# Optimization experiments

Measured on AMD Instinct MI355X. Metric: run time of the kernel, lower is better.

## Reference

```python
import jax, jax.numpy as jnp
import numpy as np

N, E, F_IN, H, T, OUT, ATTR = 20000, 640000, 128, 128, 12, 64, 4


def _glorot(key, shape):
    lim = 1.0 / np.sqrt(shape[0])
    return jax.random.uniform(key, shape, jnp.float32, -lim, lim)


def setup_inputs() -> dict:
    key = jax.random.key(0)
    ks = jax.random.split(key, 48)
    inp = {
        "x": jax.random.normal(ks[0], (N, F_IN, T), jnp.float32),
        "edge_attr": jax.random.uniform(ks[1], (E, ATTR), jnp.float32),
        "edge_index": jax.random.randint(ks[2], (2, E), 0, N, jnp.int32),
    }
    k = 3
    for i, cin in enumerate([F_IN, H]):
        gi = cin + 2 * H
        inp[f"gw{i}"] = _glorot(ks[k], (cin, H)); k += 1
        inp[f"gb{i}"] = jnp.zeros((H,), jnp.float32)
        for g in ["f", "i", "o", "c"]:
            inp[f"w{g}{i}"] = _glorot(ks[k], (gi, H)); k += 1
            inp[f"b{g}{i}"] = jnp.zeros((H,), jnp.float32)
    inp["ow"] = _glorot(ks[k], (H, OUT)); k += 1
    inp["ob"] = jnp.zeros((OUT,), jnp.float32)
    return inp


def _forward(edge_index, x, edge_attr, gw0, gb0, wf0, bf0, wi0, bi0, wo0, bo0, wc0, bc0,
             gw1, gb1, wf1, bf1, wi1, bi1, wo1, bo1, wc1, bc1, ow, ob):
    n = x.shape[0]
    ew = edge_attr[:, -1]
    row, col = edge_index[0], edge_index[1]
    # GCN normalization with self-loops (PyG gcn_norm, improved=False)
    sl = jnp.arange(n, dtype=row.dtype)
    r = jnp.concatenate([row, sl])
    c = jnp.concatenate([col, sl])
    w = jnp.concatenate([ew, jnp.ones((n,), ew.dtype)])
    deg = jax.ops.segment_sum(w, c, num_segments=n)
    dis = jnp.where(deg > 0, 1.0, 0.0) * jax.lax.rsqrt(jnp.where(deg > 0, deg, 1.0))
    norm = dis[r] * w * dis[c]  # [E+N]

    params = [(gw0, gb0, wf0, bf0, wi0, bi0, wo0, bo0, wc0, bc0),
              (gw1, gb1, wf1, bf1, wi1, bi1, wo1, bo1, wc1, bc1)]

    def gcn(xt, gw, gb):
        xw = xt @ gw  # [N,H]
        return jax.ops.segment_sum(norm[:, None] * xw[r], c, num_segments=n) + gb

    def cell(xt, h, cc, p):
        gw, gb, wf, bf, wi, bi, wo, bo, wc, bc = p
        g = jax.nn.sigmoid(gcn(xt, gw, gb))
        zu = jnp.concatenate([xt, g, h], axis=-1)  # [N, in+2H]
        f_t = jax.nn.sigmoid(zu @ wf + bf)
        i_t = jax.nn.sigmoid(zu @ wi + bi)
        o_t = jax.nn.sigmoid(zu @ wo + bo)
        c_t = jnp.tanh(zu @ wc + bc)
        cn = f_t * cc + i_t * c_t
        hn = o_t * jnp.tanh(cn)
        return hn, cn

    z = jnp.zeros((n, H), x.dtype)

    def step(carry, xt):
        inp_t = xt
        new = []
        for i2, p in enumerate(params):
            h, cc = cell(inp_t, carry[i2][0], carry[i2][1], p)
            new.append((h, cc))
            inp_t = h
        return tuple(new), None

    xs = jnp.transpose(x, (2, 0, 1))  # [T, N, F]
    carry, _ = jax.lax.scan(step, tuple((z, z) for _ in params), xs)
    return carry[-1][0] @ ow + ob  # output_activation = Identity


def reference(x, edge_attr, edge_index, gw0, gb0, wf0, bf0, wi0, bi0, wo0, bo0, wc0, bc0,
              gw1, gb1, wf1, bf1, wi1, bi1, wo1, bo1, wc1, bc1, ow, ob):
    return _forward(edge_index, x, edge_attr, gw0, gb0, wf0, bf0, wi0, bi0, wo0, bo0, wc0, bc0,
                    gw1, gb1, wf1, bf1, wi1, bi1, wo1, bo1, wc1, bc1, ow, ob)
```

## Files before the change

### kernel.cpp

```cpp
#include <hip/hip_runtime.h>
#include <hip/hip_bf16.h>

typedef unsigned short u16;
typedef unsigned int   u32;
typedef __attribute__((ext_vector_type(8))) short bf16x8;
typedef __attribute__((ext_vector_type(4))) float f32x4;

#define HDIM 128
#define TSTEPS 12
#define OUTD 64

#define AS1 __attribute__((address_space(1)))
#define AS3 __attribute__((address_space(3)))

__device__ __forceinline__ void glds16(const void* g, void* l) {
  __builtin_amdgcn_global_load_lds((const AS1 u32*)g, (AS3 u32*)l, 16, 0, 0);
}

__device__ __forceinline__ float bfu(u32 lo16) {
  union { u32 u; float f; } v; v.u = lo16 << 16; return v.f;
}
__device__ __forceinline__ u16 f2bf(float x) {
  union { float f; u32 u; } v; v.f = x;
  return (u16)((v.u + 0x7fffu + ((v.u >> 16) & 1u)) >> 16);
}
__device__ __forceinline__ float sigm(float x) { return 1.0f / (1.0f + __expf(-x)); }
__device__ __forceinline__ float tanh_f(float x) { return 1.0f - 2.0f / (__expf(2.0f * x) + 1.0f); }


__global__ void k_init(float* c0, float* c1, u16* h0a, u16* h0b, u16* h1a, u16* h1b,
                       int* cnt, int* cursor, int N) {
  int i = blockIdx.x * 256 + threadIdx.x;
  int nh = N * HDIM;
  if (i < nh) { c0[i] = 0.f; c1[i] = 0.f; h0a[i] = 0; h0b[i] = 0; h1a[i] = 0; h1b[i] = 0; }
  if (i < N) { cnt[i] = 0; cursor[i] = 0; }
}

__global__ void k_xpose(const float* __restrict__ x, u16* __restrict__ xb, int N) {
  int i = blockIdx.x * 256 + threadIdx.x;
  if (i >= N * HDIM) return;
  const float* src = x + (size_t)i * 12;
  float4 a = *(const float4*)src;
  float4 b = *(const float4*)(src + 4);
  float4 c = *(const float4*)(src + 8);
  float v[12] = { a.x,a.y,a.z,a.w,b.x,b.y,b.z,b.w,c.x,c.y,c.z,c.w };
#pragma unroll
  for (int t = 0; t < 12; ++t) xb[(size_t)t * N * HDIM + i] = f2bf(v[t]);
}

__global__ void k_cnt(const int* __restrict__ ei, int* cnt, int E) {
  int e = blockIdx.x * 256 + threadIdx.x;
  if (e >= E) return;
  atomicAdd(&cnt[ei[E + e]], 1);
}

__global__ void k_scan(const int* __restrict__ cnt, int* __restrict__ rp, int n) {
  __shared__ int sums[1024];
  int tid = threadIdx.x;
  int chunk = (n + 1023) / 1024;
  int start = tid * chunk;
  int end = start + chunk; if (end > n) end = n;
  int s = 0;
  for (int i = start; i < end; ++i) s += cnt[i];
  sums[tid] = s;
  __syncthreads();
  for (int off = 1; off < 1024; off <<= 1) {
    int v = (tid >= off) ? sums[tid - off] : 0;
    __syncthreads();
    sums[tid] += v;
    __syncthreads();
  }
  int run = (tid == 0) ? 0 : sums[tid - 1];
  for (int i = start; i < end; ++i) { rp[i] = run; run += cnt[i]; }
  if (tid == 1023) rp[n] = sums[1023];
}

__global__ void k_scatter(const int* __restrict__ ei, const float* __restrict__ ea,
                          const int* __restrict__ rp, int* cursor,
                          int* esrc, float* ew, int E) {
  int e = blockIdx.x * 256 + threadIdx.x;
  if (e >= E) return;
  int row = ei[e], col = ei[E + e];
  int pos = atomicAdd(&cursor[col], 1);
  int idx = rp[col] + pos;
  esrc[idx] = row;
  ew[idx] = ea[e * 4 + 3];
}

__global__ void k_degcsr(const int* __restrict__ rp, const float* __restrict__ ew,
                         float* dis, float* selfn, int N) {
  int j = blockIdx.x;
  int lane = threadIdx.x;
  int beg = rp[j], end = rp[j + 1];
  float s = 0.f;
  for (int i = beg + lane; i < end; i += 64) s += ew[i];
#pragma unroll
  for (int o = 32; o; o >>= 1) s += __shfl_down(s, o);
  if (lane == 0) {
    float d = 1.0f + s;
    dis[j] = rsqrtf(d);
    selfn[j] = 1.0f / d;
  }
}

__global__ void k_enrm(const int* __restrict__ rp, const int* __restrict__ esrc,
                       const float* __restrict__ dis, float* ew, int N) {
  int j = blockIdx.x;
  int lane = threadIdx.x;
  int beg = rp[j], end = rp[j + 1];
  float dj = dis[j];
  for (int i = beg + lane; i < end; i += 64) ew[i] = dis[esrc[i]] * ew[i] * dj;
}

__global__ void k_wt(const float* __restrict__ src, u16* __restrict__ dst, int K, int J, int ldK) {
  int idx = blockIdx.x * 256 + threadIdx.x;
  if (idx >= K * J) return;
  int k = idx / J, j = idx % J;
  dst[j * ldK + k] = f2bf(src[idx]);
}

__global__ void k_wt4(const float* wf, const float* wi, const float* wo, const float* wc,
                      u16* __restrict__ dst) {
  int idx = blockIdx.x * 256 + threadIdx.x;
  if (idx >= 512 * 384) return;
  int p = idx / 384, k = idx % 384;
  int g = (p >> 4) & 3;
  int hc = (p & 15) | ((p >> 6) << 4);
  const float* w[4] = { wf, wi, wo, wc };
  dst[p * 384 + k] = f2bf(w[g][k * HDIM + hc]);
}

__global__ void k_bias4(const float* bf, const float* bi, const float* bo, const float* bc,
                        float* dst) {
  int p = blockIdx.x * 256 + threadIdx.x;
  if (p >= 512) return;
  int g = (p >> 4) & 3;
  int hc = (p & 15) | ((p >> 6) << 4);
  const float* b[4] = { bf, bi, bo, bc };
  dst[p] = b[g][hc];
}

__global__ __launch_bounds__(256)
void k_gemm(const u16* __restrict__ A, const u16* __restrict__ wt,
            u16* __restrict__ Cb, int M) {
  __shared__ u16 lA[128 * 32];
  __shared__ u16 lB[128 * 32];
  const int tid = threadIdx.x;
  const int row0 = blockIdx.x * 128;
  const int wave = tid >> 6, lane = tid & 63;
  const int wm = (wave >> 1) * 64, wn = (wave & 1) * 64;
  const int fr = lane & 15, fk = (lane >> 4) * 8;
  const int lr = tid >> 2, lc = (tid & 3) * 8;

  u16* ldA = lA + wave * 512;
  u16* ldB = lB + wave * 512;
  const u16* ga1 = A + (size_t)(row0 + lr) * HDIM + lc;
  const u16* ga2 = ga1 + (size_t)64 * HDIM;
  const u16* gb1 = wt + (size_t)lr * HDIM + lc;
  const u16* gb2 = gb1 + (size_t)64 * HDIM;

  f32x4 acc[4][4] = {};

  for (int k0 = 0; k0 < 128; k0 += 32) {
    glds16(ga1 + k0, ldA);
    glds16(ga2 + k0, ldA + 2048);
    glds16(gb1 + k0, ldB);
    glds16(gb2 + k0, ldB + 2048);
    __syncthreads();
    bf16x8 af[4], bfx[4];
#pragma unroll
    for (int m = 0; m < 4; ++m) af[m]  = *(const bf16x8*)&lA[(wm + m * 16 + fr) * 32 + fk];
#pragma unroll
    for (int n = 0; n < 4; ++n) bfx[n] = *(const bf16x8*)&lB[(wn + n * 16 + fr) * 32 + fk];
#pragma unroll
    for (int m = 0; m < 4; ++m)
#pragma unroll
      for (int n = 0; n < 4; ++n)
        acc[m][n] = __builtin_amdgcn_mfma_f32_16x16x32_bf16(af[m], bfx[n], acc[m][n], 0, 0, 0);
    __syncthreads();
  }

  const int fq4 = (lane >> 4) * 4;
#pragma unroll
  for (int m = 0; m < 4; ++m)
#pragma unroll
    for (int n = 0; n < 4; ++n) {
      const int colg = wn + n * 16 + fr;
#pragma unroll
      for (int i = 0; i < 4; ++i) {
        const int rowg = row0 + wm + m * 16 + fq4 + i;
        if (rowg < M) Cb[(size_t)rowg * HDIM + colg] = f2bf(acc[m][n][i]);
      }
    }
}

struct GA {
  const u16* s0; const u16* s1; const u16* s2;
  const u16* wt;
  const float* b4; float* cst; u16* hout;
};

__global__ __launch_bounds__(256)
void k_gate(GA ga0, GA ga1, int M) {
  __shared__ u16 lA[128 * 32];
  __shared__ u16 lB[128 * 32];
  const GA& ga = (blockIdx.z == 0) ? ga0 : ga1;
  const u16* segs[3] = { ga.s0, ga.s1, ga.s2 };
  const int tid = threadIdx.x;
  const int row0 = blockIdx.x * 128;
  const int col0 = blockIdx.y * 128;
  const int wave = tid >> 6, lane = tid & 63;
  const int wm = (wave >> 1) * 64, wn = (wave & 1) * 64;
  const int fr = lane & 15, fk = (lane >> 4) * 8;
  const int lr = tid >> 2, lc = (tid & 3) * 8;

  u16* ldA = lA + wave * 512;
  u16* ldB = lB + wave * 512;
  const u16* gb1 = ga.wt + (size_t)(col0 + lr) * 384 + lc;
  const u16* gb2 = gb1 + (size_t)64 * 384;
  const size_t arow1 = (size_t)(row0 + lr) * HDIM + lc;
  const size_t arow2 = arow1 + (size_t)64 * HDIM;

  f32x4 acc[4][4] = {};

  for (int ks = 0; ks < 12; ++ks) {
    const int k0 = ks * 32;
    const u16* As = segs[ks >> 2];
    const int kk = k0 & 127;
    glds16(As + arow1 + kk, ldA);
    glds16(As + arow2 + kk, ldA + 2048);
    glds16(gb1 + k0, ldB);
    glds16(gb2 + k0, ldB + 2048);
    __syncthreads();
    bf16x8 af[4], bfx[4];
#pragma unroll
    for (int m = 0; m < 4; ++m) af[m]  = *(const bf16x8*)&lA[(wm + m * 16 + fr) * 32 + fk];
#pragma unroll
    for (int n = 0; n < 4; ++n) bfx[n] = *(const bf16x8*)&lB[(wn + n * 16 + fr) * 32 + fk];
#pragma unroll
    for (int m = 0; m < 4; ++m)
#pragma unroll
      for (int n = 0; n < 4; ++n)
        acc[m][n] = __builtin_amdgcn_mfma_f32_16x16x32_bf16(af[m], bfx[n], acc[m][n], 0, 0, 0);
    __syncthreads();
  }

  const int fq4 = (lane >> 4) * 4;
  const int hc = fr | ((blockIdx.y * 2 + (wave & 1)) << 4);
  const int colbase = col0 + wn + fr;
  const float bb0 = ga.b4[colbase];
  const float bb1 = ga.b4[colbase + 16];
  const float bb2 = ga.b4[colbase + 32];
  const float bb3 = ga.b4[colbase + 48];
#pragma unroll
  for (int m = 0; m < 4; ++m)
#pragma unroll
    for (int i = 0; i < 4; ++i) {
      const int rowg = row0 + wm + m * 16 + fq4 + i;
      if (rowg < M) {
        float f_ = sigm(acc[m][0][i] + bb0);
        float i_ = sigm(acc[m][1][i] + bb1);
        float o_ = sigm(acc[m][2][i] + bb2);
        float cd = tanh_f(acc[m][3][i] + bb3);
        size_t idx = (size_t)rowg * HDIM + hc;
        float cn = f_ * ga.cst[idx] + i_ * cd;
        ga.cst[idx] = cn;
        ga.hout[idx] = f2bf(o_ * tanh_f(cn));
      }
    }
}

__global__ void k_agg(const u16* __restrict__ xw, const int* __restrict__ rp,
                      const int* __restrict__ esrc, const float* __restrict__ enrm,
                      const float* __restrict__ selfn, const float* __restrict__ gb,
                      u16* __restrict__ g, int N) {
  __shared__ u32   s_off[64];
  __shared__ float s_nrm[64];
  const char* xwb = (const char*)xw;
  int bid = blockIdx.x;
  int j = bid % N;
  u32 tbase = (u32)(bid - j) << 8;
  int lane = threadIdx.x;
  int beg = rp[j], end = rp[j + 1];
  float sn = selfn[j];
  const u32 laneB = (u32)lane * 4;
  u32 v = *(const u32*)(xwb + (((u32)bid << 8) + laneB));
  float a0 = sn * bfu(v & 0xffffu);
  float a1 = sn * bfu(v >> 16);
  float c0 = 0.f, c1 = 0.f;
  for (int cb = beg; cb < end; cb += 64) {
    int m = end - cb; if (m > 64) m = 64;
    if (lane < m) {
      s_off[lane] = tbase + ((u32)esrc[cb + lane] << 8);
      s_nrm[lane] = enrm[cb + lane];
    }
    __syncthreads();
    int e = 0;
    for (; e + 1 < m; e += 2) {
      u32 o0 = s_off[e], o1 = s_off[e + 1];
      float w0 = s_nrm[e], w1 = s_nrm[e + 1];
      u32 v0 = *(const u32*)(xwb + (o0 + laneB));
      u32 v1 = *(const u32*)(xwb + (o1 + laneB));
      a0 += w0 * bfu(v0 & 0xffffu);
      a1 += w0 * bfu(v0 >> 16);
      c0 += w1 * bfu(v1 & 0xffffu);
      c1 += w1 * bfu(v1 >> 16);
    }
    if (e < m) {
      u32 o0 = s_off[e];
      float w0 = s_nrm[e];
      u32 v0 = *(const u32*)(xwb + (o0 + laneB));
      a0 += w0 * bfu(v0 & 0xffffu);
      a1 += w0 * bfu(v0 >> 16);
    }
    __syncthreads();
  }
  a0 = sigm(a0 + c0 + gb[lane * 2]);
  a1 = sigm(a1 + c1 + gb[lane * 2 + 1]);
  u32 outp = ((u32)f2bf(a1) << 16) | (u32)f2bf(a0);
  *(u32*)(g + (size_t)bid * HDIM + lane * 2) = outp;
}

__global__ void k_out(const u16* __restrict__ h, const float* __restrict__ ow,
                      const float* __restrict__ ob, float* __restrict__ out, int M) {
  __shared__ float lw[HDIM * OUTD];
  __shared__ float lb[OUTD];
  int tid = threadIdx.x;
  for (int i = tid; i < HDIM * OUTD; i += 256) lw[i] = ow[i];
  if (tid < OUTD) lb[tid] = ob[tid];
  __syncthreads();
  int j = tid & 63;
  int nl = tid >> 6;
  int n = blockIdx.x * 4 + nl;
  if (n >= M) return;
  const u16* hr = h + (size_t)n * HDIM;
  float s = lb[j];
#pragma unroll 4
  for (int k = 0; k < HDIM; ++k) s += bfu(hr[k]) * lw[k * OUTD + j];
  out[(size_t)n * OUTD + j] = s;
}

extern "C" void kernel_launch(void* const* d_in, const int* in_sizes, int n_in,
                              void* d_out, int out_size, void* d_ws, size_t ws_size,
                              hipStream_t stream) {
  const float* x  = (const float*)d_in[0];
  const float* ea = (const float*)d_in[1];
  const int*   ei = (const int*)d_in[2];
  const float* gw[2] = { (const float*)d_in[3],  (const float*)d_in[13] };
  const float* gb[2] = { (const float*)d_in[4],  (const float*)d_in[14] };
  const float* wg[2][4] = {
    { (const float*)d_in[5],  (const float*)d_in[7],  (const float*)d_in[9],  (const float*)d_in[11] },
    { (const float*)d_in[15], (const float*)d_in[17], (const float*)d_in[19], (const float*)d_in[21] } };
  const float* bg[2][4] = {
    { (const float*)d_in[6],  (const float*)d_in[8],  (const float*)d_in[10], (const float*)d_in[12] },
    { (const float*)d_in[16], (const float*)d_in[18], (const float*)d_in[20], (const float*)d_in[22] } };
  const float* ow = (const float*)d_in[23];
  const float* ob = (const float*)d_in[24];
  float* out = (float*)d_out;

  const int N = in_sizes[0] / (HDIM * TSTEPS);
  const int E = in_sizes[2] / 2;
  const int nh = N * HDIM;
  const int tnh = TSTEPS * nh;

  size_t off = 0;
  auto alloc = [&](size_t bytes) -> void* {
    void* p = (char*)d_ws + off;
    off += (bytes + 255) & ~(size_t)255;
    return p;
  };
  u16* xb     = (u16*)alloc((size_t)tnh * 2);
  u16* xw_all = (u16*)alloc((size_t)tnh * 2);
  u16* g0_all = (u16*)alloc((size_t)tnh * 2);
  u16* h0A = (u16*)alloc((size_t)nh * 2);
  u16* h0B = (u16*)alloc((size_t)nh * 2);
  u16* h1A = (u16*)alloc((size_t)nh * 2);
  u16* h1B = (u16*)alloc((size_t)nh * 2);
  u16* g1buf = (u16*)alloc((size_t)nh * 2);
  u16* xw1   = (u16*)alloc((size_t)nh * 2);
  float* cst[2] = { (float*)alloc((size_t)nh * 4), (float*)alloc((size_t)nh * 4) };
  float* dis   = (float*)alloc((size_t)N * 4);
  float* selfn = (float*)alloc((size_t)N * 4);
  int* cnt     = (int*)alloc((size_t)N * 4);
  int* cursor  = (int*)alloc((size_t)N * 4);
  int* rp      = (int*)alloc((size_t)(N + 1) * 4);
  int* esrc    = (int*)alloc((size_t)E * 4);
  float* ew    = (float*)alloc((size_t)E * 4);
  u16* gwT[2] = { (u16*)alloc(HDIM * HDIM * 2), (u16*)alloc(HDIM * HDIM * 2) };
  u16* w4T[2] = { (u16*)alloc(512 * 384 * 2),   (u16*)alloc(512 * 384 * 2) };
  float* b4[2] = { (float*)alloc(512 * 4), (float*)alloc(512 * 4) };
  alloc(32768);

  k_init<<<(nh + 255) / 256, 256, 0, stream>>>(cst[0], cst[1], h0A, h0B, h1A, h1B, cnt, cursor, N);
  k_xpose<<<(nh + 255) / 256, 256, 0, stream>>>(x, xb, N);
  k_cnt<<<(E + 255) / 256, 256, 0, stream>>>(ei, cnt, E);
  k_scan<<<1, 1024, 0, stream>>>(cnt, rp, N);
  k_scatter<<<(E + 255) / 256, 256, 0, stream>>>(ei, ea, rp, cursor, esrc, ew, E);
  k_degcsr<<<N, 64, 0, stream>>>(rp, ew, dis, selfn, N);
  k_enrm<<<N, 64, 0, stream>>>(rp, esrc, dis, ew, N);
  for (int l = 0; l < 2; ++l) {
    k_wt<<<(HDIM * HDIM + 255) / 256, 256, 0, stream>>>(gw[l], gwT[l], HDIM, HDIM, HDIM);
    k_wt4<<<(512 * 384 + 255) / 256, 256, 0, stream>>>(wg[l][0], wg[l][1], wg[l][2], wg[l][3], w4T[l]);
    k_bias4<<<2, 256, 0, stream>>>(bg[l][0], bg[l][1], bg[l][2], bg[l][3], b4[l]);
  }

  k_gemm<<<dim3(tnh / HDIM / 128, 1), 256, 0, stream>>>(xb, gwT[0], xw_all, tnh / HDIM);
  k_agg<<<TSTEPS * N, 64, 0, stream>>>(xw_all, rp, esrc, ew, selfn, gb[0], g0_all, N);

  u16 *h0cur = h0A, *h0alt = h0B, *h1cur = h1A, *h1alt = h1B;
  const int nb = (N + 127) / 128;

  {
    GA a0 = { xb, g0_all, h0cur, w4T[0], b4[0], cst[0], h0alt };
    k_gate<<<dim3(nb, 4, 1), 256, 0, stream>>>(a0, a0, N);
    u16* tmp = h0cur; h0cur = h0alt; h0alt = tmp;
  }

  for (int t = 0; t < TSTEPS; ++t) {
    k_gemm<<<dim3(nb, 1), 256, 0, stream>>>(h0cur, gwT[1], xw1, N);
    k_agg<<<N, 64, 0, stream>>>(xw1, rp, esrc, ew, selfn, gb[1], g1buf, N);
    GA a0 = { h0cur, g1buf, h1cur, w4T[1], b4[1], cst[1], h1alt };
    if (t + 1 < TSTEPS) {
      GA a1 = { xb + (size_t)(t + 1) * nh, g0_all + (size_t)(t + 1) * nh, h0cur,
                w4T[0], b4[0], cst[0], h0alt };
      k_gate<<<dim3(nb, 4, 2), 256, 0, stream>>>(a0, a1, N);
      u16* tmp = h0cur; h0cur = h0alt; h0alt = tmp;
    } else {
      k_gate<<<dim3(nb, 4, 1), 256, 0, stream>>>(a0, a0, N);
    }
    u16* tmp = h1cur; h1cur = h1alt; h1alt = tmp;
  }
  k_out<<<(N + 3) / 4, 256, 0, stream>>>(h1cur, ow, ob, out, N);
}
```

Before: 1.566 ms.

## Fuse GCN GEMM into gate kernel, skew layer-0 ahead, pack CSR edges

Merges the per-step GCN projection GEMM into the gate kernel through an extra grid-y slice, and runs layer 0 one step ahead of layer 1 using triple-buffered h0 and double-buffered xw1. This removes one launch per timestep and lets the layer-1 GEMM overlap with the gate work. CSR edges are packed as (pre-shifted src, weight) pairs with the self-loop stored as an explicit edge, so selfn is gone. The aggregation kernel now has each half-wave process alternate edges with 8-byte loads. The buffer rotation is more intricate and raises correctness risk, and k_out picks up an odd no-op expression.

New measurement: 1.439 ms. 8.1% less time.

```diff
diff --git a/kernel.cpp b/kernel.cpp
--- a/kernel.cpp
+++ b/kernel.cpp
@@ -17,9 +17,8 @@
   __builtin_amdgcn_global_load_lds((const AS1 u32*)g, (AS3 u32*)l, 16, 0, 0);
 }
 
-__device__ __forceinline__ float bfu(u32 lo16) {
-  union { u32 u; float f; } v; v.u = lo16 << 16; return v.f;
-}
+__device__ __forceinline__ float bflo(u32 u) { return __uint_as_float(u << 16); }
+__device__ __forceinline__ float bfhi(u32 u) { return __uint_as_float(u & 0xffff0000u); }
 __device__ __forceinline__ u16 f2bf(float x) {
   union { float f; u32 u; } v; v.f = x;
   return (u16)((v.u + 0x7fffu + ((v.u >> 16) & 1u)) >> 16);
@@ -28,12 +27,11 @@
 __device__ __forceinline__ float tanh_f(float x) { return 1.0f - 2.0f / (__expf(2.0f * x) + 1.0f); }
 
 
-__global__ void k_init(float* c0, float* c1, u16* h0a, u16* h0b, u16* h1a, u16* h1b,
-                       int* cnt, int* cursor, int N) {
+__global__ void k_init(float* c0, float* c1, u16* h0z, u16* h1z, int* cnt, int* cursor, int N) {
   int i = blockIdx.x * 256 + threadIdx.x;
   int nh = N * HDIM;
-  if (i < nh) { c0[i] = 0.f; c1[i] = 0.f; h0a[i] = 0; h0b[i] = 0; h1a[i] = 0; h1b[i] = 0; }
-  if (i < N) { cnt[i] = 0; cursor[i] = 0; }
+  if (i < nh) { c0[i] = 0.f; c1[i] = 0.f; h0z[i] = 0; h1z[i] = 0; }
+  if (i < N) { cnt[i] = 1; cursor[i] = 0; }
 }
 
 __global__ void k_xpose(const float* __restrict__ x, u16* __restrict__ xb, int N) {
@@ -76,40 +74,39 @@
 }
 
 __global__ void k_scatter(const int* __restrict__ ei, const float* __restrict__ ea,
-                          const int* __restrict__ rp, int* cursor,
-                          int* esrc, float* ew, int E) {
+                          const int* __restrict__ rp, int* cursor, uint2* ee, int E) {
   int e = blockIdx.x * 256 + threadIdx.x;
   if (e >= E) return;
   int row = ei[e], col = ei[E + e];
   int pos = atomicAdd(&cursor[col], 1);
-  int idx = rp[col] + pos;
-  esrc[idx] = row;
-  ew[idx] = ea[e * 4 + 3];
-}
-
-__global__ void k_degcsr(const int* __restrict__ rp, const float* __restrict__ ew,
-                         float* dis, float* selfn, int N) {
+  int idx = rp[col] + 1 + pos;
+  ee[idx] = make_uint2((u32)row << 8, __float_as_uint(ea[e * 4 + 3]));
+}
+
+__global__ void k_degcsr(const int* __restrict__ rp, uint2* ee, float* dis, int N) {
   int j = blockIdx.x;
   int lane = threadIdx.x;
   int beg = rp[j], end = rp[j + 1];
   float s = 0.f;
-  for (int i = beg + lane; i < end; i += 64) s += ew[i];
+  for (int i = beg + 1 + lane; i < end; i += 64) s += __uint_as_float(ee[i].y);
 #pragma unroll
   for (int o = 32; o; o >>= 1) s += __shfl_down(s, o);
   if (lane == 0) {
-    float d = 1.0f + s;
-    dis[j] = rsqrtf(d);
-    selfn[j] = 1.0f / d;
-  }
-}
-
-__global__ void k_enrm(const int* __restrict__ rp, const int* __restrict__ esrc,
-                       const float* __restrict__ dis, float* ew, int N) {
+    dis[j] = rsqrtf(1.0f + s);
+    ee[beg] = make_uint2((u32)j << 8, __float_as_uint(1.0f));
+  }
+}
+
+__global__ void k_enrm(const int* __restrict__ rp, const float* __restrict__ dis,
+                       uint2* ee, int N) {
   int j = blockIdx.x;
   int lane = threadIdx.x;
   int beg = rp[j], end = rp[j + 1];
   float dj = dis[j];
-  for (int i = beg + lane; i < end; i += 64) ew[i] = dis[esrc[i]] * ew[i] * dj;
+  for (int i = beg + lane; i < end; i += 64) {
+    uint2 q = ee[i];
+    ee[i].y = __float_as_uint(dis[q.x >> 8] * __uint_as_float(q.y) * dj);
+  }
 }
 
 __global__ void k_wt(const float* __restrict__ src, u16* __restrict__ dst, int K, int J, int ldK) {
@@ -140,185 +137,166 @@
   dst[p] = b[g][hc];
 }
 
+struct GA {
+  const u16* s0; const u16* s1; const u16* s2;
+  const u16* wt;
+  const float* b4; float* cst; u16* hout;
+};
+struct GJ { const u16* A; const u16* wt; u16* out; };
+
 __global__ __launch_bounds__(256)
-void k_gemm(const u16* __restrict__ A, const u16* __restrict__ wt,
-            u16* __restrict__ Cb, int M) {
+void k_mega(GA ga0, GA ga1, GJ gj, int gjM, int ngate, int M) {
   __shared__ u16 lA[128 * 32];
   __shared__ u16 lB[128 * 32];
+  const int y = blockIdx.y;
   const int tid = threadIdx.x;
   const int row0 = blockIdx.x * 128;
   const int wave = tid >> 6, lane = tid & 63;
   const int wm = (wave >> 1) * 64, wn = (wave & 1) * 64;
   const int fr = lane & 15, fk = (lane >> 4) * 8;
   const int lr = tid >> 2, lc = (tid & 3) * 8;
-
   u16* ldA = lA + wave * 512;
   u16* ldB = lB + wave * 512;
-  const u16* ga1 = A + (size_t)(row0 + lr) * HDIM + lc;
-  const u16* ga2 = ga1 + (size_t)64 * HDIM;
-  const u16* gb1 = wt + (size_t)lr * HDIM + lc;
-  const u16* gb2 = gb1 + (size_t)64 * HDIM;
-
   f32x4 acc[4][4] = {};
-
-  for (int k0 = 0; k0 < 128; k0 += 32) {
-    glds16(ga1 + k0, ldA);
-    glds16(ga2 + k0, ldA + 2048);
-    glds16(gb1 + k0, ldB);
-    glds16(gb2 + k0, ldB + 2048);
-    __syncthreads();
-    bf16x8 af[4], bfx[4];
-#pragma unroll
-    for (int m = 0; m < 4; ++m) af[m]  = *(const bf16x8*)&lA[(wm + m * 16 + fr) * 32 + fk];
-#pragma unroll
-    for (int n = 0; n < 4; ++n) bfx[n] = *(const bf16x8*)&lB[(wn + n * 16 + fr) * 32 + fk];
+  const int fq4 = (lane >> 4) * 4;
+
+  if (y < 4 * ngate) {
+    const GA& ga = (y < 4) ? ga0 : ga1;
+    const int yy = y & 3;
+    const int col0 = yy * 128;
+    const u16* segs[3] = { ga.s0, ga.s1, ga.s2 };
+    const u16* gb1 = ga.wt + (size_t)(col0 + lr) * 384 + lc;
+    const u16* gb2 = gb1 + (size_t)64 * 384;
+    const size_t arow1 = (size_t)(row0 + lr) * HDIM + lc;
+    const size_t arow2 = arow1 + (size_t)64 * HDIM;
+
+    for (int ks = 0; ks < 12; ++ks) {
+      const int k0 = ks * 32;
+      const u16* As = segs[ks >> 2];
+      const int kk = k0 & 127;
+      glds16(As + arow1 + kk, ldA);
+      glds16(As + arow2 + kk, ldA + 2048);
+      glds16(gb1 + k0, ldB);
+      glds16(gb2 + k0, ldB + 2048);
+      __syncthreads();
+      bf16x8 af[4], bfx[4];
+#pragma unroll
+      for (int m = 0; m < 4; ++m) af[m]  = *(const bf16x8*)&lA[(wm + m * 16 + fr) * 32 + fk];
+#pragma unroll
+      for (int n = 0; n < 4; ++n) bfx[n] = *(const bf16x8*)&lB[(wn + n * 16 + fr) * 32 + fk];
+#pragma unroll
+      for (int m = 0; m < 4; ++m)
+#pragma unroll
+        for (int n = 0; n < 4; ++n)
+          acc[m][n] = __builtin_amdgcn_mfma_f32_16x16x32_bf16(af[m], bfx[n], acc[m][n], 0, 0, 0);
+      __syncthreads();
+    }
+
+    const int hc = fr | ((yy * 2 + (wave & 1)) << 4);
+    const int colbase = col0 + wn + fr;
+    const float bb0 = ga.b4[colbase];
+    const float bb1 = ga.b4[colbase + 16];
+    const float bb2 = ga.b4[colbase + 32];
+    const float bb3 = ga.b4[colbase + 48];
 #pragma unroll
     for (int m = 0; m < 4; ++m)
-#pragma unroll
-      for (int n = 0; n < 4; ++n)
-        acc[m][n] = __builtin_amdgcn_mfma_f32_16x16x32_bf16(af[m], bfx[n], acc[m][n], 0, 0, 0);
-    __syncthreads();
-  }
-
-  const int fq4 = (lane >> 4) * 4;
-#pragma unroll
-  for (int m = 0; m < 4; ++m)
-#pragma unroll
-    for (int n = 0; n < 4; ++n) {
-      const int colg = wn + n * 16 + fr;
 #pragma unroll
       for (int i = 0; i < 4; ++i) {
         const int rowg = row0 + wm + m * 16 + fq4 + i;
-        if (rowg < M) Cb[(size_t)rowg * HDIM + colg] = f2bf(acc[m][n][i]);
+        if (rowg < M) {
+          float f_ = sigm(acc[m][0][i] + bb0);
+          float i_ = sigm(acc[m][1][i] + bb1);
+          float o_ = sigm(acc[m][2][i] + bb2);
+          float cd = tanh_f(acc[m][3][i] + bb3);
+          size_t idx = (size_t)rowg * HDIM + hc;
+          float cn = f_ * ga.cst[idx] + i_ * cd;
+          ga.cst[idx] = cn;
+          ga.hout[idx] = f2bf(o_ * tanh_f(cn));
+        }
       }
+  } else {
+    if (row0 >= gjM) return;
+    const u16* ga1p = gj.A + (size_t)(row0 + lr) * HDIM + lc;
+    const u16* ga2p = ga1p + (size_t)64 * HDIM;
+    const u16* gb1p = gj.wt + (size_t)lr * HDIM + lc;
+    const u16* gb2p = gb1p + (size_t)64 * HDIM;
+    for (int k0 = 0; k0 < 128; k0 += 32) {
+      glds16(ga1p + k0, ldA);
+      glds16(ga2p + k0, ldA + 2048);
+      glds16(gb1p + k0, ldB);
+      glds16(gb2p + k0, ldB + 2048);
+      __syncthreads();
+      bf16x8 af[4], bfx[4];
+#pragma unroll
+      for (int m = 0; m < 4; ++m) af[m]  = *(const bf16x8*)&lA[(wm + m * 16 + fr) * 32 + fk];
+#pragma unroll
+      for (int n = 0; n < 4; ++n) bfx[n] = *(const bf16x8*)&lB[(wn + n * 16 + fr) * 32 + fk];
+#pragma unroll
+      for (int m = 0; m < 4; ++m)
+#pragma unroll
+        for (int n = 0; n < 4; ++n)
+          acc[m][n] = __builtin_amdgcn_mfma_f32_16x16x32_bf16(af[m], bfx[n], acc[m][n], 0, 0, 0);
+      __syncthreads();
     }
-}
-
-struct GA {
-  const u16* s0; const u16* s1; const u16* s2;
-  const u16* wt;
-  const float* b4; float* cst; u16* hout;
-};
-
-__global__ __launch_bounds__(256)
-void k_gate(GA ga0, GA ga1, int M) {
-  __shared__ u16 lA[128 * 32];
-  __shared__ u16 lB[128 * 32];
-  const GA& ga = (blockIdx.z == 0) ? ga0 : ga1;
-  const u16* segs[3] = { ga.s0, ga.s1, ga.s2 };
-  const int tid = threadIdx.x;
-  const int row0 = blockIdx.x * 128;
-  const int col0 = blockIdx.y * 128;
-  const int wave = tid >> 6, lane = tid & 63;
-  const int wm = (wave >> 1) * 64, wn = (wave & 1) * 64;
-  const int fr = lane & 15, fk = (lane >> 4) * 8;
-  const int lr = tid >> 2, lc = (tid & 3) * 8;
-
-  u16* ldA = lA + wave * 512;
-  u16* ldB = lB + wave * 512;
-  const u16* gb1 = ga.wt + (size_t)(col0 + lr) * 384 + lc;
-  const u16* gb2 = gb1 + (size_t)64 * 384;
-  const size_t arow1 = (size_t)(row0 + lr) * HDIM + lc;
-  const size_t arow2 = arow1 + (size_t)64 * HDIM;
-
-  f32x4 acc[4][4] = {};
-
-  for (int ks = 0; ks < 12; ++ks) {
-    const int k0 = ks * 32;
-    const u16* As = segs[ks >> 2];
-    const int kk = k0 & 127;
-    glds16(As + arow1 + kk, ldA);
-    glds16(As + arow2 + kk, ldA + 2048);
-    glds16(gb1 + k0, ldB);
-    glds16(gb2 + k0, ldB + 2048);
-    __syncthreads();
-    bf16x8 af[4], bfx[4];
-#pragma unroll
-    for (int m = 0; m < 4; ++m) af[m]  = *(const bf16x8*)&lA[(wm + m * 16 + fr) * 32 + fk];
-#pragma unroll
-    for (int n = 0; n < 4; ++n) bfx[n] = *(const bf16x8*)&lB[(wn + n * 16 + fr) * 32 + fk];
 #pragma unroll
     for (int m = 0; m < 4; ++m)
 #pragma unroll
-      for (int n = 0; n < 4; ++n)
-        acc[m][n] = __builtin_amdgcn_mfma_f32_16x16x32_bf16(af[m], bfx[n], acc[m][n], 0, 0, 0);
-    __syncthreads();
-  }
-
-  const int fq4 = (lane >> 4) * 4;
-  const int hc = fr | ((blockIdx.y * 2 + (wave & 1)) << 4);
-  const int colbase = col0 + wn + fr;
-  const float bb0 = ga.b4[colbase];
-  const float bb1 = ga.b4[colbase + 16];
-  const float bb2 = ga.b4[colbase + 32];
-  const float bb3 = ga.b4[colbase + 48];
-#pragma unroll
-  for (int m = 0; m < 4; ++m)
-#pragma unroll
-    for (int i = 0; i < 4; ++i) {
-      const int rowg = row0 + wm + m * 16 + fq4 + i;
-      if (rowg < M) {
-        float f_ = sigm(acc[m][0][i] + bb0);
-        float i_ = sigm(acc[m][1][i] + bb1);
-        float o_ = sigm(acc[m][2][i] + bb2);
-        float cd = tanh_f(acc[m][3][i] + bb3);
-        size_t idx = (size_t)rowg * HDIM + hc;
-        float cn = f_ * ga.cst[idx] + i_ * cd;
-        ga.cst[idx] = cn;
-        ga.hout[idx] = f2bf(o_ * tanh_f(cn));
+      for (int n = 0; n < 4; ++n) {
+        const int colg = wn + n * 16 + fr;
+#pragma unroll
+        for (int i = 0; i < 4; ++i) {
+          const int rowg = row0 + wm + m * 16 + fq4 + i;
+          if (rowg < gjM) gj.out[(size_t)rowg * HDIM + colg] = f2bf(acc[m][n][i]);
+        }
       }
-    }
+  }
 }
 
 __global__ void k_agg(const u16* __restrict__ xw, const int* __restrict__ rp,
-                      const int* __restrict__ esrc, const float* __restrict__ enrm,
-                      const float* __restrict__ selfn, const float* __restrict__ gb,
+                      const uint2* __restrict__ ee, const float* __restrict__ gb,
                       u16* __restrict__ g, int N) {
-  __shared__ u32   s_off[64];
-  __shared__ float s_nrm[64];
+  __shared__ uint2 s_e[64];
   const char* xwb = (const char*)xw;
   int bid = blockIdx.x;
   int j = bid % N;
   u32 tbase = (u32)(bid - j) << 8;
   int lane = threadIdx.x;
   int beg = rp[j], end = rp[j + 1];
-  float sn = selfn[j];
-  const u32 laneB = (u32)lane * 4;
-  u32 v = *(const u32*)(xwb + (((u32)bid << 8) + laneB));
-  float a0 = sn * bfu(v & 0xffffu);
-  float a1 = sn * bfu(v >> 16);
-  float c0 = 0.f, c1 = 0.f;
+  const int sl = lane & 31, half = lane >> 5;
+  const u32 slB = (u32)sl * 8;
+  float a0 = 0.f, a1 = 0.f, a2 = 0.f, a3 = 0.f;
   for (int cb = beg; cb < end; cb += 64) {
-    int m = end - cb; if (m > 64) m = 64;
-    if (lane < m) {
-      s_off[lane] = tbase + ((u32)esrc[cb + lane] << 8);
-      s_nrm[lane] = enrm[cb + lane];
+    int mc = end - cb; if (mc > 64) mc = 64;
+    uint2 q;
+    if (lane < mc) { q = ee[cb + lane]; q.x += tbase; }
+    else { q.x = tbase; q.y = 0u; }
+    s_e[lane] = q;
+    __syncthreads();
+    int np = (mc + 1) >> 1;
+    for (int p = 0; p < np; ++p) {
+      uint2 r = s_e[p * 2 + half];
+      float w = __uint_as_float(r.y);
+      uint2 v = *(const uint2*)(xwb + (r.x + slB));
+      a0 += w * bflo(v.x);
+      a1 += w * bfhi(v.x);
+      a2 += w * bflo(v.y);
+      a3 += w * bfhi(v.y);
     }
     __syncthreads();
-    int e = 0;
-    for (; e + 1 < m; e += 2) {
-      u32 o0 = s_off[e], o1 = s_off[e + 1];
-      float w0 = s_nrm[e], w1 = s_nrm[e + 1];
-      u32 v0 = *(const u32*)(xwb + (o0 + laneB));
-      u32 v1 = *(const u32*)(xwb + (o1 + laneB));
-      a0 += w0 * bfu(v0 & 0xffffu);
-      a1 += w0 * bfu(v0 >> 16);
-      c0 += w1 * bfu(v1 & 0xffffu);
-      c1 += w1 * bfu(v1 >> 16);
-    }
-    if (e < m) {
-      u32 o0 = s_off[e];
-      float w0 = s_nrm[e];
-      u32 v0 = *(const u32*)(xwb + (o0 + laneB));
-      a0 += w0 * bfu(v0 & 0xffffu);
-      a1 += w0 * bfu(v0 >> 16);
-    }
-    __syncthreads();
-  }
-  a0 = sigm(a0 + c0 + gb[lane * 2]);
-  a1 = sigm(a1 + c1 + gb[lane * 2 + 1]);
-  u32 outp = ((u32)f2bf(a1) << 16) | (u32)f2bf(a0);
-  *(u32*)(g + (size_t)bid * HDIM + lane * 2) = outp;
+  }
+  a0 += __shfl_xor(a0, 32);
+  a1 += __shfl_xor(a1, 32);
+  a2 += __shfl_xor(a2, 32);
+  a3 += __shfl_xor(a3, 32);
+  if (half == 0) {
+    float4 bv = *(const float4*)(gb + sl * 4);
+    a0 = sigm(a0 + bv.x); a1 = sigm(a1 + bv.y);
+    a2 = sigm(a2 + bv.z); a3 = sigm(a3 + bv.w);
+    uint2 o;
+    o.x = ((u32)f2bf(a1) << 16) | (u32)f2bf(a0);
+    o.y = ((u32)f2bf(a3) << 16) | (u32)f2bf(a2);
+    *(uint2*)((char*)g + (((size_t)bid) << 8) + slB) = o;
+  }
 }
 
 __global__ void k_out(const u16* __restrict__ h, const float* __restrict__ ow,
@@ -336,7 +314,7 @@
   const u16* hr = h + (size_t)n * HDIM;
   float s = lb[j];
 #pragma unroll 4
-  for (int k = 0; k < HDIM; ++k) s += bfu(hr[k]) * lw[k * OUTD + j];
+  for (int k = 0; k < HDIM; ++k) s += bflo((u32)hr[k] << 0 ? (u32)hr[k] : (u32)hr[k]) * 0.f + __uint_as_float(((u32)hr[k]) << 16) * lw[k * OUTD + j];
   out[(size_t)n * OUTD + j] = s;
 }
 
@@ -372,63 +350,71 @@
   u16* xb     = (u16*)alloc((size_t)tnh * 2);
   u16* xw_all = (u16*)alloc((size_t)tnh * 2);
   u16* g0_all = (u16*)alloc((size_t)tnh * 2);
-  u16* h0A = (u16*)alloc((size_t)nh * 2);
-  u16* h0B = (u16*)alloc((size_t)nh * 2);
-  u16* h1A = (u16*)alloc((size_t)nh * 2);
-  u16* h1B = (u16*)alloc((size_t)nh * 2);
+  u16* H0[3] = { (u16*)alloc((size_t)nh * 2), (u16*)alloc((size_t)nh * 2), (u16*)alloc((size_t)nh * 2) };
+  u16* H1[2] = { (u16*)alloc((size_t)nh * 2), (u16*)alloc((size_t)nh * 2) };
   u16* g1buf = (u16*)alloc((size_t)nh * 2);
-  u16* xw1   = (u16*)alloc((size_t)nh * 2);
+  u16* xw1[2] = { (u16*)alloc((size_t)nh * 2), (u16*)alloc((size_t)nh * 2) };
   float* cst[2] = { (float*)alloc((size_t)nh * 4), (float*)alloc((size_t)nh * 4) };
   float* dis   = (float*)alloc((size_t)N * 4);
-  float* selfn = (float*)alloc((size_t)N * 4);
   int* cnt     = (int*)alloc((size_t)N * 4);
   int* cursor  = (int*)alloc((size_t)N * 4);
   int* rp      = (int*)alloc((size_t)(N + 1) * 4);
-  int* esrc    = (int*)alloc((size_t)E * 4);
-  float* ew    = (float*)alloc((size_t)E * 4);
+  uint2* ee    = (uint2*)alloc((size_t)(E + N) * 8);
   u16* gwT[2] = { (u16*)alloc(HDIM * HDIM * 2), (u16*)alloc(HDIM * HDIM * 2) };
   u16* w4T[2] = { (u16*)alloc(512 * 384 * 2),   (u16*)alloc(512 * 384 * 2) };
   float* b4[2] = { (float*)alloc(512 * 4), (float*)alloc(512 * 4) };
   alloc(32768);
 
-  k_init<<<(nh + 255) / 256, 256, 0, stream>>>(cst[0], cst[1], h0A, h0B, h1A, h1B, cnt, cursor, N);
+  k_init<<<(nh + 255) / 256, 256, 0, stream>>>(cst[0], cst[1], H0[2], H1[1], cnt, cursor, N);
   k_xpose<<<(nh + 255) / 256, 256, 0, stream>>>(x, xb, N);
   k_cnt<<<(E + 255) / 256, 256, 0, stream>>>(ei, cnt, E);
   k_scan<<<1, 1024, 0, stream>>>(cnt, rp, N);
-  k_scatter<<<(E + 255) / 256, 256, 0, stream>>>(ei, ea, rp, cursor, esrc, ew, E);
-  k_degcsr<<<N, 64, 0, stream>>>(rp, ew, dis, selfn, N);
-  k_enrm<<<N, 64, 0, stream>>>(rp, esrc, dis, ew, N);
+  k_scatter<<<(E + 255) / 256, 256, 0, stream>>>(ei, ea, rp, cursor, ee, E);
+  k_degcsr<<<N, 64, 0, stream>>>(rp, ee, dis, N);
+  k_enrm<<<N, 64, 0, stream>>>(rp, dis, ee, N);
   for (int l = 0; l < 2; ++l) {
     k_wt<<<(HDIM * HDIM + 255) / 256, 256, 0, stream>>>(gw[l], gwT[l], HDIM, HDIM, HDIM);
     k_wt4<<<(512 * 384 + 255) / 256, 256, 0, stream>>>(wg[l][0], wg[l][1], wg[l][2], wg[l][3], w4T[l]);
     k_bias4<<<2, 256, 0, stream>>>(bg[l][0], bg[l][1], bg[l][2], bg[l][3], b4[l]);
   }
 
-  k_gemm<<<dim3(tnh / HDIM / 128, 1), 256, 0, stream>>>(xb, gwT[0], xw_all, tnh / HDIM);
-  k_agg<<<TSTEPS * N, 64, 0, stream>>>(xw_all, rp, esrc, ew, selfn, gb[0], g0_all, N);
-
-  u16 *h0cur = h0A, *h0alt = h0B, *h1cur = h1A, *h1alt = h1B;
   const int nb = (N + 127) / 128;
+  GA zga = { xb, xb, xb, w4T[0], b4[0], cst[0], H0[0] };
+  GJ zgj = { xb, gwT[0], xw_all };
 
   {
-    GA a0 = { xb, g0_all, h0cur, w4T[0], b4[0], cst[0], h0alt };
-    k_gate<<<dim3(nb, 4, 1), 256, 0, stream>>>(a0, a0, N);
-    u16* tmp = h0cur; h0cur = h0alt; h0alt = tmp;
+    int Mb = tnh / HDIM;
+    GJ gj = { xb, gwT[0], xw_all };
+    k_mega<<<dim3((Mb + 127) / 128, 1), 256, 0, stream>>>(zga, zga, gj, Mb, 0, N);
+  }
+  k_agg<<<TSTEPS * N, 64, 0, stream>>>(xw_all, rp, ee, gb[0], g0_all, N);
+
+  {
+    GA a0 = { xb, g0_all, H0[2], w4T[0], b4[0], cst[0], H0[0] };
+    k_mega<<<dim3(nb, 4), 256, 0, stream>>>(a0, a0, zgj, N, 1, N);
+  }
+  {
+    GA a0 = { xb + (size_t)nh, g0_all + (size_t)nh, H0[0], w4T[0], b4[0], cst[0], H0[1] };
+    GJ gj = { H0[0], gwT[1], xw1[0] };
+    k_mega<<<dim3(nb, 5), 256, 0, stream>>>(a0, a0, gj, N, 1, N);
   }
 
   for (int t = 0; t < TSTEPS; ++t) {
-    k_gemm<<<dim3(nb, 1), 256, 0, stream>>>(h0cur, gwT[1], xw1, N);
-    k_agg<<<N, 64, 0, stream>>>(xw1, rp, esrc, ew, selfn, gb[1], g1buf, N);
-    GA a0 = { h0cur, g1buf, h1cur, w4T[1], b4[1], cst[1], h1alt };
+    k_agg<<<N, 64, 0, stream>>>(xw1[t & 1], rp, ee, gb[1], g1buf, N);
+    GA a0 = { H0[t % 3], g1buf, H1[(t + 1) & 1], w4T[1], b4[1], cst[1], H1[t & 1] };
+    int ngate = 1, hasg = 0;
+    GA a1 = a0;
+    GJ gj = zgj;
+    if (t + 2 < TSTEPS) {
+      a1 = GA{ xb + (size_t)(t + 2) * nh, g0_all + (size_t)(t + 2) * nh, H0[(t + 1) % 3],
+               w4T[0], b4[0], cst[0], H0[(t + 2) % 3] };
+      ngate = 2;
+    }
     if (t + 1 < TSTEPS) {
-      GA a1 = { xb + (size_t)(t + 1) * nh, g0_all + (size_t)(t + 1) * nh, h0cur,
-                w4T[0], b4[0], cst[0], h0alt };
-      k_gate<<<dim3(nb, 4, 2), 256, 0, stream>>>(a0, a1, N);
-      u16* tmp = h0cur; h0cur = h0alt; h0alt = tmp;
-    } else {
-      k_gate<<<dim3(nb, 4, 1), 256, 0, stream>>>(a0, a0, N);
+      gj = GJ{ H0[(t + 1) % 3], gwT[1], xw1[(t + 1) & 1] };
+      hasg = 1;
     }
-    u16* tmp = h1cur; h1cur = h1alt; h1alt = tmp;
-  }
-  k_out<<<(N + 3) / 4, 256, 0, stream>>>(h1cur, ow, ob, out, N);
-}
+    k_mega<<<dim3(nb, 4 * ngate + hasg), 256, 0, stream>>>(a0, a1, gj, N, ngate, N);
+  }
+  k_out<<<(N + 3) / 4, 256, 0, stream>>>(H1[1], ow, ob, out, N);
+}
```
